# Kernel optimization log

Measured on AMD Instinct MI355X. Metric: run time of the kernel, lower is better.

## Reference

```python
import jax, jax.numpy as jnp
import numpy as np

NEG_BIG = -9e15
ALPHA = 0.2  # leakyrelu negative slope


def setup_inputs() -> dict:
    key = jax.random.key(0)
    k1, k2, k3, k4 = jax.random.split(key, 4)
    N, F_in, F_out = 8192, 256, 256
    h = jax.random.normal(k1, (N, F_in), dtype=jnp.float32)
    adj = jax.random.randint(k2, (N, N), 0, 2).astype(jnp.float32)
    W = jax.random.normal(k3, (F_in, F_out), dtype=jnp.float32) * (1.414 / np.sqrt(F_in))
    a = jax.random.normal(k4, (2 * F_out, 1), dtype=jnp.float32) * (1.414 / np.sqrt(2 * F_out))
    return {"h": h, "adj": adj, "W": W, "a": a}


def reference(h, adj, W, a):
    F_out = W.shape[1]
    Wh = h @ W  # [N, F_out]
    # Decomposed additive score: e_ij = leakyrelu(a1.Wh_i + a2.Wh_j)
    # identical to matmul(cat([Wh_i, Wh_j]), a) in the original.
    a1 = a[:F_out, 0]  # [F_out]
    a2 = a[F_out:, 0]  # [F_out]
    s1 = Wh @ a1  # [N]
    s2 = Wh @ a2  # [N]
    e = jax.nn.leaky_relu(s1[:, None] + s2[None, :], negative_slope=ALPHA)  # [N, N]
    e = jnp.where(adj > 0, e, NEG_BIG)
    attention = jax.nn.softmax(e, axis=1)
    # dropout skipped (eval mode: training=False)
    h_prime = attention @ Wh  # [N, F_out]
    return jax.nn.elu(h_prime)
```

## Files before the change

kernel.cpp:

```cpp
#include <hip/hip_runtime.h>
#include <hip/hip_bf16.h>

#define N 8192
#define F 256
#define KSPLIT 4
#define JBLK (N / KSPLIT)
#define NITER (JBLK / 64)

using s16x8 = __attribute__((ext_vector_type(8))) short;
using f32x4 = __attribute__((ext_vector_type(4))) float;

static __device__ __forceinline__ unsigned short f2bf(float f) {
  unsigned int u = __float_as_uint(f);
  unsigned int r = u + 0x7fffu + ((u >> 16) & 1u);
  return (unsigned short)(r >> 16);
}
static __device__ __forceinline__ float bf2f(unsigned short u) {
  return __uint_as_float(((unsigned int)u) << 16);
}

__global__ __launch_bounds__(256) void k0_wt(const float* __restrict__ W,
                                             unsigned short* __restrict__ Wt) {
  int k = blockIdx.x;
  int f = threadIdx.x;
  Wt[f * 256 + k] = f2bf(W[k * 256 + f]);
}

__global__ __launch_bounds__(256) void k1_wh(const float* __restrict__ h,
                                             const unsigned short* __restrict__ Wt,
                                             unsigned short* __restrict__ WhbT) {
  __shared__ char lds[8192 + 32768];
  char* Alds = lds;
  char* Blds = lds + 8192;
  int t = threadIdx.x;
  int i0 = blockIdx.x * 64;
  int l = t & 63, w = t >> 6;
  int lr = l & 15, lk = l >> 4;
  f32x4 acc[4][4] = {};
  for (int kt = 0; kt < 4; ++kt) {
    int k0 = kt * 64;
    if (kt) __syncthreads();
#pragma unroll
    for (int c = 0; c < 4; ++c) {
      int flat = c * 256 + t;
      int i = flat >> 4, jc = flat & 15;
      float4 v = *reinterpret_cast<const float4*>(h + (size_t)(i0 + i) * 256 + k0 + jc * 4);
      ushort4 pk;
      pk.x = f2bf(v.x); pk.y = f2bf(v.y); pk.z = f2bf(v.z); pk.w = f2bf(v.w);
      *reinterpret_cast<ushort4*>(Alds + i * 128 + ((jc * 8) ^ ((i & 7) << 4))) = pk;
    }
#pragma unroll
    for (int c = 0; c < 8; ++c) {
      int idx = c * 256 + t;
      int fr = idx >> 3, kc = idx & 7;
      uint4 v = *reinterpret_cast<const uint4*>(Wt + fr * 256 + k0 + kc * 8);
      *reinterpret_cast<uint4*>(Blds + fr * 128 + ((kc * 16) ^ ((fr & 7) << 4))) = v;
    }
    __syncthreads();
#pragma unroll
    for (int kk = 0; kk < 2; ++kk) {
      int kofs = kk * 64 + lk * 16;
      s16x8 afr[4], bfr[4];
#pragma unroll
      for (int mf = 0; mf < 4; ++mf) {
        int ar = mf * 16 + lr;
        afr[mf] = *reinterpret_cast<const s16x8*>(Alds + ar * 128 + (kofs ^ ((ar & 7) << 4)));
      }
#pragma unroll
      for (int nf = 0; nf < 4; ++nf) {
        int br = w * 64 + nf * 16 + lr;
        bfr[nf] = *reinterpret_cast<const s16x8*>(Blds + br * 128 + (kofs ^ ((br & 7) << 4)));
      }
#pragma unroll
      for (int mf = 0; mf < 4; ++mf)
#pragma unroll
        for (int nf = 0; nf < 4; ++nf)
          acc[mf][nf] = __builtin_amdgcn_mfma_f32_16x16x32_bf16(afr[mf], bfr[nf], acc[mf][nf], 0, 0, 0);
    }
  }
#pragma unroll
  for (int mf = 0; mf < 4; ++mf) {
#pragma unroll
    for (int nf = 0; nf < 4; ++nf) {
      int f = w * 64 + nf * 16 + lr;
      int j = i0 + mf * 16 + lk * 4;
      ushort4 pk;
      pk.x = f2bf(acc[mf][nf][0]);
      pk.y = f2bf(acc[mf][nf][1]);
      pk.z = f2bf(acc[mf][nf][2]);
      pk.w = f2bf(acc[mf][nf][3]);
      *reinterpret_cast<ushort4*>(WhbT + (size_t)f * N + j) = pk;
    }
  }
}

__global__ __launch_bounds__(256) void k2_s(const unsigned short* __restrict__ WhbT,
                                            const float* __restrict__ a,
                                            float* __restrict__ s1,
                                            float* __restrict__ s2) {
  int j = blockIdx.x * 256 + threadIdx.x;
  float acc1 = 0.f, acc2 = 0.f;
#pragma unroll 8
  for (int f = 0; f < 256; ++f) {
    float v = bf2f(WhbT[(size_t)f * N + j]);
    acc1 += v * a[f];
    acc2 += v * a[256 + f];
  }
  s1[j] = acc1;
  s2[j] = acc2;
}

__global__ __launch_bounds__(256, 2) void k3_attn(const float* __restrict__ adj,
                                                  const unsigned short* __restrict__ WhbT,
                                                  const float* __restrict__ s1,
                                                  const float* __restrict__ s2,
                                                  float* __restrict__ numw,
                                                  float* __restrict__ denw) {
  __shared__ char Bbuf[2 * 32768];
  int t = threadIdx.x;
  int wv = t >> 6;
  int l = t & 63;
  int lr = l & 15, lk = l >> 4;
  int i0 = blockIdx.x * 64;
  int ks = blockIdx.y;
  int jb = ks * JBLK;
  int row = i0 + wv * 16 + lr;
  const float* arow = adj + (size_t)row * N + jb;
  const float* s2b = s2 + jb;
  float s1v = s1[row];
  int lko = lk * 8;

  f32x4 acc[16] = {};
  float dsum = 0.f;

  float4 ajc[4], svc[4], ajn[4], svn[4];
  uint4 bvn[8];

#pragma unroll
  for (int kk = 0; kk < 2; ++kk)
#pragma unroll
    for (int h = 0; h < 2; ++h) {
      ajc[kk * 2 + h] = *reinterpret_cast<const float4*>(arow + kk * 32 + lko + h * 4);
      svc[kk * 2 + h] = *reinterpret_cast<const float4*>(s2b + kk * 32 + lko + h * 4);
    }
#pragma unroll
  for (int c = 0; c < 8; ++c) {
    int idx = c * 256 + t;
    int fr = idx >> 3, kc = idx & 7;
    bvn[c] = *reinterpret_cast<const uint4*>(WhbT + (size_t)fr * N + jb + kc * 8);
  }
#pragma unroll
  for (int c = 0; c < 8; ++c) {
    int idx = c * 256 + t;
    int fr = idx >> 3, kc = idx & 7;
    *reinterpret_cast<uint4*>(Bbuf + fr * 128 + ((kc * 16) ^ ((fr & 7) << 4))) = bvn[c];
  }
  __syncthreads();

  for (int it = 0; it < NITER; ++it) {
    bool pf = (it + 1 < NITER);
    if (pf) {
      int jn = (it + 1) * 64;
#pragma unroll
      for (int kk = 0; kk < 2; ++kk)
#pragma unroll
        for (int h = 0; h < 2; ++h)
          ajn[kk * 2 + h] = *reinterpret_cast<const float4*>(arow + jn + kk * 32 + lko + h * 4);
#pragma unroll
      for (int c = 0; c < 8; ++c) {
        int idx = c * 256 + t;
        int fr = idx >> 3, kc = idx & 7;
        bvn[c] = *reinterpret_cast<const uint4*>(WhbT + (size_t)fr * N + jb + jn + kc * 8);
      }
#pragma unroll
      for (int kk = 0; kk < 2; ++kk)
#pragma unroll
        for (int h = 0; h < 2; ++h)
          svn[kk * 2 + h] = *reinterpret_cast<const float4*>(s2b + jn + kk * 32 + lko + h * 4);
    }
    s16x8 afr[2];
#pragma unroll
    for (int kk = 0; kk < 2; ++kk) {
      unsigned short u[8];
#pragma unroll
      for (int h = 0; h < 2; ++h) {
        float4 av = ajc[kk * 2 + h];
        float4 tv = svc[kk * 2 + h];
        float x;
        x = s1v + tv.x; x = fmaxf(x, 0.2f * x); u[h * 4 + 0] = av.x > 0.f ? f2bf(__expf(x)) : 0;
        x = s1v + tv.y; x = fmaxf(x, 0.2f * x); u[h * 4 + 1] = av.y > 0.f ? f2bf(__expf(x)) : 0;
        x = s1v + tv.z; x = fmaxf(x, 0.2f * x); u[h * 4 + 2] = av.z > 0.f ? f2bf(__expf(x)) : 0;
        x = s1v + tv.w; x = fmaxf(x, 0.2f * x); u[h * 4 + 3] = av.w > 0.f ? f2bf(__expf(x)) : 0;
      }
      s16x8 af;
#pragma unroll
      for (int e = 0; e < 8; ++e) {
        af[e] = (short)u[e];
        dsum += bf2f(u[e]);
      }
      afr[kk] = af;
    }
    const char* B = Bbuf + (it & 1) * 32768;
#pragma unroll
    for (int kk = 0; kk < 2; ++kk) {
      int kofs = kk * 64 + lk * 16;
#pragma unroll
      for (int nf = 0; nf < 16; ++nf) {
        int br = nf * 16 + lr;
        s16x8 bfr = *reinterpret_cast<const s16x8*>(B + br * 128 + (kofs ^ ((br & 7) << 4)));
        acc[nf] = __builtin_amdgcn_mfma_f32_16x16x32_bf16(afr[kk], bfr, acc[nf], 0, 0, 0);
      }
    }
    if (pf) {
      char* B1 = Bbuf + ((it + 1) & 1) * 32768;
#pragma unroll
      for (int c = 0; c < 8; ++c) {
        int idx = c * 256 + t;
        int fr = idx >> 3, kc = idx & 7;
        *reinterpret_cast<uint4*>(B1 + fr * 128 + ((kc * 16) ^ ((fr & 7) << 4))) = bvn[c];
      }
    }
    __syncthreads();
    if (pf) {
#pragma unroll
      for (int q = 0; q < 4; ++q) { ajc[q] = ajn[q]; svc[q] = svn[q]; }
    }
  }

  dsum += __shfl_xor(dsum, 16);
  dsum += __shfl_xor(dsum, 32);
  if (l < 16) denw[(size_t)ks * N + row] = dsum;

  float* nump = numw + (size_t)ks * N * F;
#pragma unroll
  for (int nf = 0; nf < 16; ++nf) {
#pragma unroll
    for (int r = 0; r < 4; ++r) {
      nump[(size_t)(i0 + wv * 16 + lk * 4 + r) * F + nf * 16 + lr] = acc[nf][r];
    }
  }
}

__global__ __launch_bounds__(256) void k4_fin(const float* __restrict__ numw,
                                              const float* __restrict__ denw,
                                              float* __restrict__ out) {
  int idx = (blockIdx.x * 256 + threadIdx.x) * 4;
  int i = idx >> 8;
  float4 sn = {0.f, 0.f, 0.f, 0.f};
  float sd = 0.f;
#pragma unroll
  for (int ksp = 0; ksp < KSPLIT; ++ksp) {
    float4 v = *reinterpret_cast<const float4*>(numw + (size_t)ksp * N * F + idx);
    sn.x += v.x; sn.y += v.y; sn.z += v.z; sn.w += v.w;
    sd += denw[ksp * N + i];
  }
  float r = 1.f / sd;
  float4 o;
  float hp;
  hp = sn.x * r; o.x = hp > 0.f ? hp : (__expf(hp) - 1.f);
  hp = sn.y * r; o.y = hp > 0.f ? hp : (__expf(hp) - 1.f);
  hp = sn.z * r; o.z = hp > 0.f ? hp : (__expf(hp) - 1.f);
  hp = sn.w * r; o.w = hp > 0.f ? hp : (__expf(hp) - 1.f);
  *reinterpret_cast<float4*>(out + idx) = o;
}

extern "C" void kernel_launch(void* const* d_in, const int* in_sizes, int n_in,
                              void* d_out, int out_size, void* d_ws, size_t ws_size,
                              hipStream_t stream) {
  const float* h   = (const float*)d_in[0];
  const float* adj = (const float*)d_in[1];
  const float* W   = (const float*)d_in[2];
  const float* a   = (const float*)d_in[3];
  float* out = (float*)d_out;

  char* ws = (char*)d_ws;
  size_t o = 0;
  unsigned short* WhbT = (unsigned short*)(ws + o); o += (size_t)4 * 1024 * 1024;
  float* s1            = (float*)(ws + o); o += 32768;
  float* s2            = (float*)(ws + o); o += 32768;
  float* denw          = (float*)(ws + o); o += 131072;
  unsigned short* Wt   = (unsigned short*)(ws + o); o += 131072;
  float* numw          = (float*)(ws + o); o += (size_t)KSPLIT * N * F * 4;

  hipLaunchKernelGGL(k0_wt, dim3(256), dim3(256), 0, stream, W, Wt);
  hipLaunchKernelGGL(k1_wh, dim3(N / 64), dim3(256), 0, stream, h, Wt, WhbT);
  hipLaunchKernelGGL(k2_s, dim3(N / 256), dim3(256), 0, stream, WhbT, a, s1, s2);
  hipLaunchKernelGGL(k3_attn, dim3(128, KSPLIT), dim3(256), 0, stream,
                     adj, WhbT, s1, s2, numw, denw);
  hipLaunchKernelGGL(k4_fin, dim3(N * F / 1024), dim3(256), 0, stream, numw, denw, out);
}
```

Before: 146.8 us.

## Unroll attention loop by two with ping-pong adj/s2 registers and raw barriers

Restructures the attention main loop into a two-tile unrolled ping-pong schedule. adj and s2 values are prefetched two tiles ahead into alternating register sets, and the register copies at the end of each iteration are removed. The __syncthreads is replaced with an LDS-only waitcnt, s_barrier and sched_barrier, so outstanding global loads no longer have to drain at each barrier. The launch_bounds occupancy hint of 2 is also dropped, which allows more registers but may reduce occupancy.

```diff
diff --git a/kernel.cpp b/kernel.cpp
--- a/kernel.cpp
+++ b/kernel.cpp
@@ -110,12 +110,12 @@
   s2[j] = acc2;
 }
 
-__global__ __launch_bounds__(256, 2) void k3_attn(const float* __restrict__ adj,
-                                                  const unsigned short* __restrict__ WhbT,
-                                                  const float* __restrict__ s1,
-                                                  const float* __restrict__ s2,
-                                                  float* __restrict__ numw,
-                                                  float* __restrict__ denw) {
+__global__ __launch_bounds__(256) void k3_attn(const float* __restrict__ adj,
+                                               const unsigned short* __restrict__ WhbT,
+                                               const float* __restrict__ s1,
+                                               const float* __restrict__ s2,
+                                               float* __restrict__ numw,
+                                               float* __restrict__ denw) {
   __shared__ char Bbuf[2 * 32768];
   int t = threadIdx.x;
   int wv = t >> 6;
@@ -133,98 +133,108 @@
   f32x4 acc[16] = {};
   float dsum = 0.f;
 
-  float4 ajc[4], svc[4], ajn[4], svn[4];
+  float4 aj0[4], aj1[4], sv0[4], sv1[4];
   uint4 bvn[8];
 
-#pragma unroll
-  for (int kk = 0; kk < 2; ++kk)
-#pragma unroll
-    for (int h = 0; h < 2; ++h) {
-      ajc[kk * 2 + h] = *reinterpret_cast<const float4*>(arow + kk * 32 + lko + h * 4);
-      svc[kk * 2 + h] = *reinterpret_cast<const float4*>(s2b + kk * 32 + lko + h * 4);
-    }
-#pragma unroll
-  for (int c = 0; c < 8; ++c) {
-    int idx = c * 256 + t;
-    int fr = idx >> 3, kc = idx & 7;
-    bvn[c] = *reinterpret_cast<const uint4*>(WhbT + (size_t)fr * N + jb + kc * 8);
-  }
-#pragma unroll
-  for (int c = 0; c < 8; ++c) {
-    int idx = c * 256 + t;
-    int fr = idx >> 3, kc = idx & 7;
-    *reinterpret_cast<uint4*>(Bbuf + fr * 128 + ((kc * 16) ^ ((fr & 7) << 4))) = bvn[c];
-  }
-  __syncthreads();
-
-  for (int it = 0; it < NITER; ++it) {
-    bool pf = (it + 1 < NITER);
-    if (pf) {
-      int jn = (it + 1) * 64;
-#pragma unroll
-      for (int kk = 0; kk < 2; ++kk)
-#pragma unroll
-        for (int h = 0; h < 2; ++h)
-          ajn[kk * 2 + h] = *reinterpret_cast<const float4*>(arow + jn + kk * 32 + lko + h * 4);
-#pragma unroll
-      for (int c = 0; c < 8; ++c) {
-        int idx = c * 256 + t;
-        int fr = idx >> 3, kc = idx & 7;
-        bvn[c] = *reinterpret_cast<const uint4*>(WhbT + (size_t)fr * N + jb + jn + kc * 8);
-      }
-#pragma unroll
-      for (int kk = 0; kk < 2; ++kk)
-#pragma unroll
-        for (int h = 0; h < 2; ++h)
-          svn[kk * 2 + h] = *reinterpret_cast<const float4*>(s2b + jn + kk * 32 + lko + h * 4);
-    }
-    s16x8 afr[2];
-#pragma unroll
-    for (int kk = 0; kk < 2; ++kk) {
-      unsigned short u[8];
-#pragma unroll
-      for (int h = 0; h < 2; ++h) {
-        float4 av = ajc[kk * 2 + h];
-        float4 tv = svc[kk * 2 + h];
-        float x;
-        x = s1v + tv.x; x = fmaxf(x, 0.2f * x); u[h * 4 + 0] = av.x > 0.f ? f2bf(__expf(x)) : 0;
-        x = s1v + tv.y; x = fmaxf(x, 0.2f * x); u[h * 4 + 1] = av.y > 0.f ? f2bf(__expf(x)) : 0;
-        x = s1v + tv.z; x = fmaxf(x, 0.2f * x); u[h * 4 + 2] = av.z > 0.f ? f2bf(__expf(x)) : 0;
-        x = s1v + tv.w; x = fmaxf(x, 0.2f * x); u[h * 4 + 3] = av.w > 0.f ? f2bf(__expf(x)) : 0;
-      }
-      s16x8 af;
-#pragma unroll
-      for (int e = 0; e < 8; ++e) {
-        af[e] = (short)u[e];
-        dsum += bf2f(u[e]);
-      }
-      afr[kk] = af;
-    }
-    const char* B = Bbuf + (it & 1) * 32768;
-#pragma unroll
-    for (int kk = 0; kk < 2; ++kk) {
-      int kofs = kk * 64 + lk * 16;
-#pragma unroll
-      for (int nf = 0; nf < 16; ++nf) {
-        int br = nf * 16 + lr;
-        s16x8 bfr = *reinterpret_cast<const s16x8*>(B + br * 128 + (kofs ^ ((br & 7) << 4)));
-        acc[nf] = __builtin_amdgcn_mfma_f32_16x16x32_bf16(afr[kk], bfr, acc[nf], 0, 0, 0);
-      }
-    }
-    if (pf) {
-      char* B1 = Bbuf + ((it + 1) & 1) * 32768;
-#pragma unroll
-      for (int c = 0; c < 8; ++c) {
-        int idx = c * 256 + t;
-        int fr = idx >> 3, kc = idx & 7;
-        *reinterpret_cast<uint4*>(B1 + fr * 128 + ((kc * 16) ^ ((fr & 7) << 4))) = bvn[c];
-      }
-    }
-    __syncthreads();
-    if (pf) {
-#pragma unroll
-      for (int q = 0; q < 4; ++q) { ajc[q] = ajn[q]; svc[q] = svn[q]; }
-    }
+#define LOAD_AJ(dst, tile)                                                      \
+  {                                                                             \
+    int jn = (tile) * 64;                                                       \
+    _Pragma("unroll") for (int kk = 0; kk < 2; ++kk)                            \
+        _Pragma("unroll") for (int h = 0; h < 2; ++h)                           \
+            dst[kk * 2 + h] =                                                   \
+        *reinterpret_cast<const float4*>(arow + jn + kk * 32 + lko + h * 4);    \
+  }
+#define LOAD_SV(dst, tile)                                                      \
+  {                                                                             \
+    int jn = (tile) * 64;                                                       \
+    _Pragma("unroll") for (int kk = 0; kk < 2; ++kk)                            \
+        _Pragma("unroll") for (int h = 0; h < 2; ++h)                           \
+            dst[kk * 2 + h] =                                                   \
+        *reinterpret_cast<const float4*>(s2b + jn + kk * 32 + lko + h * 4);     \
+  }
+#define LOAD_BV(tile)                                                           \
+  {                                                                             \
+    int j0 = jb + (tile) * 64;                                                  \
+    _Pragma("unroll") for (int c = 0; c < 8; ++c) {                             \
+      int idx = c * 256 + t;                                                    \
+      int fr = idx >> 3, kc = idx & 7;                                          \
+      bvn[c] = *reinterpret_cast<const uint4*>(WhbT + (size_t)fr * N + j0 + kc * 8); \
+    }                                                                           \
+  }
+#define WRITE_BV(buf)                                                           \
+  {                                                                             \
+    char* Bw = Bbuf + (buf) * 32768;                                            \
+    _Pragma("unroll") for (int c = 0; c < 8; ++c) {                             \
+      int idx = c * 256 + t;                                                    \
+      int fr = idx >> 3, kc = idx & 7;                                          \
+      *reinterpret_cast<uint4*>(Bw + fr * 128 + ((kc * 16) ^ ((fr & 7) << 4))) = bvn[c]; \
+    }                                                                           \
+  }
+#define PCOMP(ajr, svr)                                                         \
+  {                                                                             \
+    _Pragma("unroll") for (int kk = 0; kk < 2; ++kk) {                          \
+      unsigned short u[8];                                                      \
+      _Pragma("unroll") for (int h = 0; h < 2; ++h) {                           \
+        float4 av = ajr[kk * 2 + h];                                            \
+        float4 tv = svr[kk * 2 + h];                                            \
+        float x;                                                                \
+        x = s1v + tv.x; x = fmaxf(x, 0.2f * x); u[h * 4 + 0] = av.x > 0.f ? f2bf(__expf(x)) : 0; \
+        x = s1v + tv.y; x = fmaxf(x, 0.2f * x); u[h * 4 + 1] = av.y > 0.f ? f2bf(__expf(x)) : 0; \
+        x = s1v + tv.z; x = fmaxf(x, 0.2f * x); u[h * 4 + 2] = av.z > 0.f ? f2bf(__expf(x)) : 0; \
+        x = s1v + tv.w; x = fmaxf(x, 0.2f * x); u[h * 4 + 3] = av.w > 0.f ? f2bf(__expf(x)) : 0; \
+      }                                                                         \
+      s16x8 af;                                                                 \
+      _Pragma("unroll") for (int e = 0; e < 8; ++e) {                           \
+        af[e] = (short)u[e];                                                    \
+        dsum += bf2f(u[e]);                                                     \
+      }                                                                         \
+      afr[kk] = af;                                                             \
+    }                                                                           \
+  }
+#define MFMA_TILE(buf)                                                          \
+  {                                                                             \
+    const char* Br = Bbuf + (buf) * 32768;                                      \
+    _Pragma("unroll") for (int kk = 0; kk < 2; ++kk) {                          \
+      int kofs = kk * 64 + lk * 16;                                             \
+      _Pragma("unroll") for (int nf = 0; nf < 16; ++nf) {                       \
+        int br = nf * 16 + lr;                                                  \
+        s16x8 bfr = *reinterpret_cast<const s16x8*>(Br + br * 128 + (kofs ^ ((br & 7) << 4))); \
+        acc[nf] = __builtin_amdgcn_mfma_f32_16x16x32_bf16(afr[kk], bfr, acc[nf], 0, 0, 0); \
+      }                                                                         \
+    }                                                                           \
+  }
+#define RAW_BARRIER()                                                           \
+  {                                                                             \
+    asm volatile("s_waitcnt lgkmcnt(0)" ::: "memory");                          \
+    __builtin_amdgcn_s_barrier();                                               \
+    __builtin_amdgcn_sched_barrier(0);                                          \
+  }
+
+  s16x8 afr[2];
+
+  LOAD_BV(0);
+  LOAD_SV(sv0, 0);
+  LOAD_SV(sv1, 1);
+  LOAD_AJ(aj0, 0);
+  LOAD_AJ(aj1, 1);
+  WRITE_BV(0);
+  RAW_BARRIER();
+
+  for (int k2i = 0; k2i < NITER / 2; ++k2i) {
+    int e = 2 * k2i;
+    LOAD_BV(e + 1);
+    PCOMP(aj0, sv0);
+    if (e + 2 < NITER) { LOAD_SV(sv0, e + 2); LOAD_AJ(aj0, e + 2); }
+    MFMA_TILE(0);
+    WRITE_BV(1);
+    RAW_BARRIER();
+    int o = e + 1;
+    if (o + 1 < NITER) LOAD_BV(o + 1);
+    PCOMP(aj1, sv1);
+    if (o + 2 < NITER) { LOAD_SV(sv1, o + 2); LOAD_AJ(aj1, o + 2); }
+    MFMA_TILE(1);
+    if (o + 1 < NITER) WRITE_BV(0);
+    RAW_BARRIER();
   }
 
   dsum += __shfl_xor(dsum, 16);
@@ -239,6 +249,13 @@
       nump[(size_t)(i0 + wv * 16 + lk * 4 + r) * F + nf * 16 + lr] = acc[nf][r];
     }
   }
+#undef LOAD_AJ
+#undef LOAD_SV
+#undef LOAD_BV
+#undef WRITE_BV
+#undef PCOMP
+#undef MFMA_TILE
+#undef RAW_BARRIER
 }
 
 __global__ __launch_bounds__(256) void k4_fin(const float* __restrict__ numw,
```

Result: slower. 297.6 us (+102.7%).
